# Kernel optimization log

Hardware: AMD Instinct MI355X
Metric: run time of the kernel (lower is better)

## Reference

```python
import jax, jax.numpy as jnp
import numpy as np


def setup_inputs() -> dict:
    key = jax.random.key(0)
    k1, k2 = jax.random.split(key)
    latent = jax.random.normal(k1, (131072, 128), dtype=jnp.float32)
    coords = jax.random.normal(k2, (2048, 128), dtype=jnp.float32)
    return {"latent": latent, "coords": coords}


def reference(latent, coords):
    # torch.cdist(latent, coords).min(1)[1]
    # argmin over euclidean distance == argmin over squared distance,
    # so we skip the sqrt (same result, cheaper and numerically safer).
    x2 = jnp.sum(latent * latent, axis=1, keepdims=True)          # [N, 1]
    c2 = jnp.sum(coords * coords, axis=1)                          # [C]
    cross = latent @ coords.T                                      # [N, C]
    d2 = x2 + c2[None, :] - 2.0 * cross                            # [N, C] squared dists
    return jnp.argmin(d2, axis=1)                                  # [N] int indices
```

## Files before the change

### kernel.cpp

```cpp
#include <hip/hip_runtime.h>


constexpr int D = 128;
constexpr int C = 2048;
constexpr int NCH = 64;
constexpr int NCHUNKS = C / NCH;
constexpr float MARGIN = 0.02f;
constexpr int WL_CAP = 32768;

constexpr size_t WS_CNT = 8192;
constexpr size_t WS_WL  = 16384;
constexpr size_t WS_BH  = 262144;
constexpr size_t WS_BL  = 786432;

typedef __attribute__((ext_vector_type(8))) short short8;
typedef __attribute__((ext_vector_type(4))) float f32x4;

__device__ inline unsigned short bf16_rne(float x) {
    unsigned u = __float_as_uint(x);
    u += 0x7FFFu + ((u >> 16) & 1u);
    return (unsigned short)(u >> 16);
}
__device__ inline float bf16_to_f(unsigned short h) {
    return __uint_as_float(((unsigned)h) << 16);
}
__device__ inline void split8(const float* v, short8* hi, short8* lo) {
#pragma unroll
    for (int j = 0; j < 8; ++j) {
        unsigned short h = bf16_rne(v[j]);
        (*hi)[j] = (short)h;
        (*lo)[j] = (short)bf16_rne(v[j] - bf16_to_f(h));
    }
}

__global__ void prep_coords(const float* __restrict__ coords,
                            unsigned short* __restrict__ Bh,
                            unsigned short* __restrict__ Bl,
                            float* __restrict__ c2, int* __restrict__ counter) {
    int t = blockIdx.x * blockDim.x + threadIdx.x;
    if (t == 0) *counter = 0;
    if (t >= C * 16) return;
    int c  = t >> 4;
    int k8 = t & 15;
    float v[8];
    *(float4*)(v)     = *(const float4*)(coords + (size_t)c * D + k8 * 8);
    *(float4*)(v + 4) = *(const float4*)(coords + (size_t)c * D + k8 * 8 + 4);
    short8 hi, lo;
    split8(v, &hi, &lo);
    int ch = c >> 6, nl = c & 63;
    size_t off = (size_t)ch * (NCH * 128) + ((size_t)nl * 16 + (k8 ^ (nl & 15))) * 8;
    *(short8*)(Bh + off) = hi;
    *(short8*)(Bl + off) = lo;
    float p = 0.f;
#pragma unroll
    for (int j = 0; j < 8; ++j) p = fmaf(v[j], v[j], p);
#pragma unroll
    for (int m = 1; m <= 8; m <<= 1) p += __shfl_xor(p, m, 64);
    if (k8 == 0) c2[c] = p;
}


__global__ __launch_bounds__(256, 3) void centroid_fast(
        const float* __restrict__ latent,
        const unsigned short* __restrict__ Bh_img,
        const unsigned short* __restrict__ Bl_img,
        const float* __restrict__ c2g,
        int* __restrict__ out,
        int* __restrict__ counter,
        int* __restrict__ worklist) {
    __shared__ __align__(16) unsigned short Bh[NCH * 128], Bl[NCH * 128];
    __shared__ float sc2[NCH];

    const int tid  = threadIdx.x;
    const int wid  = tid >> 6;
    const int lane = tid & 63;
    const int q    = lane >> 4, lr = lane & 15;
    const int row_block = blockIdx.x * 128;

    short8 Ah[2][4], Al[2][4];
#pragma unroll
    for (int mt = 0; mt < 2; ++mt) {
        const float* rp = latent + (size_t)(row_block + wid * 32 + mt * 16 + lr) * D;
#pragma unroll
        for (int ks = 0; ks < 4; ++ks) {
            float v[8];
            *(float4*)(v)     = *(const float4*)(rp + ks * 32 + q * 8);
            *(float4*)(v + 4) = *(const float4*)(rp + ks * 32 + q * 8 + 4);
            split8(v, &Ah[mt][ks], &Al[mt][ks]);
        }
    }

    float b1[8], b2[8];
    int   bidx[8];
#pragma unroll
    for (int s = 0; s < 8; ++s) { b1[s] = 3.4e38f; b2[s] = 3.4e38f; bidx[s] = 0; }

    for (int ch = 0; ch < NCHUNKS; ++ch) {
        __syncthreads();
        {
            const unsigned short* sh = Bh_img + (size_t)ch * (NCH * 128);
            const unsigned short* sl = Bl_img + (size_t)ch * (NCH * 128);
#pragma unroll
            for (int i = 0; i < 4; ++i) {
                int e = (i * 256 + tid) * 8;
                *(short8*)(Bh + e) = *(const short8*)(sh + e);
                *(short8*)(Bl + e) = *(const short8*)(sl + e);
            }
            if (tid < NCH) sc2[tid] = c2g[ch * NCH + tid];
        }
        __syncthreads();

#pragma unroll
        for (int nt = 0; nt < 4; ++nt) {
            const int nl = nt * 16 + lr;
            f32x4 acc[2];
#pragma unroll
            for (int mt = 0; mt < 2; ++mt) acc[mt] = (f32x4){0.f, 0.f, 0.f, 0.f};
#pragma unroll
            for (int ks = 0; ks < 4; ++ks) {
                const int xv = ((ks * 4) | q) ^ lr;
                const int e  = nl * 128 + xv * 8;
                short8 bh = *(const short8*)(Bh + e);
                short8 bl = *(const short8*)(Bl + e);
#pragma unroll
                for (int mt = 0; mt < 2; ++mt) {
                    acc[mt] = __builtin_amdgcn_mfma_f32_16x16x32_bf16(Ah[mt][ks], bh, acc[mt], 0, 0, 0);
                    acc[mt] = __builtin_amdgcn_mfma_f32_16x16x32_bf16(Ah[mt][ks], bl, acc[mt], 0, 0, 0);
                    acc[mt] = __builtin_amdgcn_mfma_f32_16x16x32_bf16(Al[mt][ks], bh, acc[mt], 0, 0, 0);
                }
            }
            const float c2v = sc2[nl];
            const int n_global = ch * NCH + nl;
#pragma unroll
            for (int mt = 0; mt < 2; ++mt)
#pragma unroll
                for (int r = 0; r < 4; ++r) {
                    int slot = mt * 4 + r;
                    float s = fmaf(-2.f, acc[mt][r], c2v);
                    bool lt = s < b1[slot];
                    float t = fmaxf(s, b1[slot]);
                    b2[slot]   = fminf(b2[slot], t);
                    b1[slot]   = fminf(s, b1[slot]);
                    bidx[slot] = lt ? n_global : bidx[slot];
                }
        }
    }

#pragma unroll
    for (int m = 1; m <= 8; m <<= 1) {
#pragma unroll
        for (int s = 0; s < 8; ++s) {
            float ob1 = __shfl_xor(b1[s], m, 64);
            float ob2 = __shfl_xor(b2[s], m, 64);
            int   oix = __shfl_xor(bidx[s], m, 64);
            float mx  = fmaxf(b1[s], ob1);
            b2[s] = fminf(fminf(b2[s], ob2), mx);
            bool take = (ob1 < b1[s]) || (ob1 == b1[s] && oix < bidx[s]);
            b1[s]   = take ? ob1 : b1[s];
            bidx[s] = take ? oix : bidx[s];
        }
    }
#pragma unroll
    for (int s = 0; s < 8; ++s) {
        if (lr == s) {
            int row = row_block + wid * 32 + (s >> 2) * 16 + q * 4 + (s & 3);
            out[row] = bidx[s];
            if (b2[s] - b1[s] < MARGIN) {
                int w = atomicAdd(counter, 1);
                if (w < WL_CAP) worklist[w] = row;
            }
        }
    }
}


__global__ __launch_bounds__(256) void refine_fp64(
        const float* __restrict__ latent, const float* __restrict__ coords,
        const int* __restrict__ worklist, const int* __restrict__ counter,
        int wl_cap, int* __restrict__ out) {
    __shared__ float  xs[D];
    __shared__ double rv[256];
    __shared__ int    ri[256];

    int n = *counter;
    if (n > wl_cap) n = wl_cap;

    for (int wi = blockIdx.x; wi < n; wi += gridDim.x) {
        int row = worklist[wi];
        if (threadIdx.x < D)
            xs[threadIdx.x] = latent[(size_t)row * D + threadIdx.x];
        __syncthreads();

        double best = 1.0e300;
        int    bix  = 0;
        for (int c = threadIdx.x; c < C; c += 256) {
            const float4* cp = (const float4*)(coords + (size_t)c * D);
            double s = 0.0;
#pragma unroll 8
            for (int k4 = 0; k4 < 32; ++k4) {
                float4 v = cp[k4];
                double d0 = (double)xs[k4 * 4 + 0] - (double)v.x;
                double d1 = (double)xs[k4 * 4 + 1] - (double)v.y;
                double d2 = (double)xs[k4 * 4 + 2] - (double)v.z;
                double d3 = (double)xs[k4 * 4 + 3] - (double)v.w;
                s = fma(d0, d0, s); s = fma(d1, d1, s);
                s = fma(d2, d2, s); s = fma(d3, d3, s);
            }
            if (s < best) { best = s; bix = c; }
        }
        rv[threadIdx.x] = best;
        ri[threadIdx.x] = bix;
        __syncthreads();
        for (int off = 128; off > 0; off >>= 1) {
            if (threadIdx.x < off) {
                double ov = rv[threadIdx.x + off];
                int    oi = ri[threadIdx.x + off];
                if (ov < rv[threadIdx.x] ||
                    (ov == rv[threadIdx.x] && oi < ri[threadIdx.x])) {
                    rv[threadIdx.x] = ov;
                    ri[threadIdx.x] = oi;
                }
            }
            __syncthreads();
        }
        if (threadIdx.x == 0) out[row] = ri[0];
        __syncthreads();
    }
}

extern "C" void kernel_launch(void* const* d_in, const int* in_sizes, int n_in,
                              void* d_out, int out_size, void* d_ws, size_t ws_size,
                              hipStream_t stream) {
    const float* latent = (const float*)d_in[0];
    const float* coords = (const float*)d_in[1];
    int*         out    = (int*)d_out;

    char* ws = (char*)d_ws;
    float* c2      = (float*)ws;
    int*   counter = (int*)(ws + WS_CNT);
    int*   wl      = (int*)(ws + WS_WL);
    unsigned short* Bh = (unsigned short*)(ws + WS_BH);
    unsigned short* Bl = (unsigned short*)(ws + WS_BL);
    const int n_rows = in_sizes[0] / D;

    prep_coords<<<(C * 16) / 256, 256, 0, stream>>>(coords, Bh, Bl, c2, counter);
    centroid_fast<<<n_rows / 128, 256, 0, stream>>>(latent, Bh, Bl, c2, out,
                                                    counter, wl);
    refine_fp64<<<608, 256, 0, stream>>>(latent, coords, wl, counter, WL_CAP, out);
}
```

Baseline: 327.3 us.

## Double-buffer coord chunks in LDS and batch four rows per refine block

The main kernel now uses two LDS buffers with half-size chunks of 32 centroids. The next chunk is prefetched into registers while the current one is computed, which removes one barrier per iteration and hides global-load latency behind MFMA work. The fp64 refine kernel now processes four worklist rows per block, reusing each coords load across four rows, and its grid shrinks from 608 to 256 blocks. This adds register pressure and more serial reductions per block, which may hurt occupancy at launch bound 3.

New measurement: 345.4 us. 1.06x slower.

```diff
diff --git a/kernel.cpp b/kernel.cpp
--- a/kernel.cpp
+++ b/kernel.cpp
@@ -3,7 +3,7 @@
 
 constexpr int D = 128;
 constexpr int C = 2048;
-constexpr int NCH = 64;
+constexpr int NCH = 32;
 constexpr int NCHUNKS = C / NCH;
 constexpr float MARGIN = 0.02f;
 constexpr int WL_CAP = 32768;
@@ -47,7 +47,7 @@
     *(float4*)(v + 4) = *(const float4*)(coords + (size_t)c * D + k8 * 8 + 4);
     short8 hi, lo;
     split8(v, &hi, &lo);
-    int ch = c >> 6, nl = c & 63;
+    int ch = c >> 5, nl = c & 31;
     size_t off = (size_t)ch * (NCH * 128) + ((size_t)nl * 16 + (k8 ^ (nl & 15))) * 8;
     *(short8*)(Bh + off) = hi;
     *(short8*)(Bl + off) = lo;
@@ -68,8 +68,8 @@
         int* __restrict__ out,
         int* __restrict__ counter,
         int* __restrict__ worklist) {
-    __shared__ __align__(16) unsigned short Bh[NCH * 128], Bl[NCH * 128];
-    __shared__ float sc2[NCH];
+    __shared__ __align__(16) unsigned short Bs[2][2][NCH * 128];
+    __shared__ float sc2[2][NCH];
 
     const int tid  = threadIdx.x;
     const int wid  = tid >> 6;
@@ -90,38 +90,50 @@
         }
     }
 
+#pragma unroll
+    for (int i = 0; i < 2; ++i) {
+        int o = (i * 256 + tid) * 8;
+        *(short8*)(&Bs[0][0][o]) = *(const short8*)(Bh_img + o);
+        *(short8*)(&Bs[0][1][o]) = *(const short8*)(Bl_img + o);
+    }
+    if (tid < NCH) sc2[0][tid] = c2g[tid];
+
     float b1[8], b2[8];
     int   bidx[8];
 #pragma unroll
     for (int s = 0; s < 8; ++s) { b1[s] = 3.4e38f; b2[s] = 3.4e38f; bidx[s] = 0; }
 
+    int buf = 0;
     for (int ch = 0; ch < NCHUNKS; ++ch) {
         __syncthreads();
-        {
-            const unsigned short* sh = Bh_img + (size_t)ch * (NCH * 128);
-            const unsigned short* sl = Bl_img + (size_t)ch * (NCH * 128);
-#pragma unroll
-            for (int i = 0; i < 4; ++i) {
-                int e = (i * 256 + tid) * 8;
-                *(short8*)(Bh + e) = *(const short8*)(sh + e);
-                *(short8*)(Bl + e) = *(const short8*)(sl + e);
-            }
-            if (tid < NCH) sc2[tid] = c2g[ch * NCH + tid];
-        }
-        __syncthreads();
-
-#pragma unroll
-        for (int nt = 0; nt < 4; ++nt) {
-            const int nl = nt * 16 + lr;
+
+        short8 nh[2], nlo[2];
+        float  nc2 = 0.f;
+        const bool more = (ch + 1 < NCHUNKS);
+        if (more) {
+            const unsigned short* sh = Bh_img + (size_t)(ch + 1) * (NCH * 128);
+            const unsigned short* sl = Bl_img + (size_t)(ch + 1) * (NCH * 128);
+#pragma unroll
+            for (int i = 0; i < 2; ++i) {
+                int o = (i * 256 + tid) * 8;
+                nh[i]  = *(const short8*)(sh + o);
+                nlo[i] = *(const short8*)(sl + o);
+            }
+            if (tid < NCH) nc2 = c2g[(ch + 1) * NCH + tid];
+        }
+
+#pragma unroll
+        for (int nt = 0; nt < 2; ++nt) {
+            const int nlc = nt * 16 + lr;
             f32x4 acc[2];
 #pragma unroll
             for (int mt = 0; mt < 2; ++mt) acc[mt] = (f32x4){0.f, 0.f, 0.f, 0.f};
 #pragma unroll
             for (int ks = 0; ks < 4; ++ks) {
                 const int xv = ((ks * 4) | q) ^ lr;
-                const int e  = nl * 128 + xv * 8;
-                short8 bh = *(const short8*)(Bh + e);
-                short8 bl = *(const short8*)(Bl + e);
+                const int e  = nlc * 128 + xv * 8;
+                short8 bh = *(const short8*)(&Bs[buf][0][e]);
+                short8 bl = *(const short8*)(&Bs[buf][1][e]);
 #pragma unroll
                 for (int mt = 0; mt < 2; ++mt) {
                     acc[mt] = __builtin_amdgcn_mfma_f32_16x16x32_bf16(Ah[mt][ks], bh, acc[mt], 0, 0, 0);
@@ -129,8 +141,8 @@
                     acc[mt] = __builtin_amdgcn_mfma_f32_16x16x32_bf16(Al[mt][ks], bh, acc[mt], 0, 0, 0);
                 }
             }
-            const float c2v = sc2[nl];
-            const int n_global = ch * NCH + nl;
+            const float c2v = sc2[buf][nlc];
+            const int n_global = ch * NCH + nlc;
 #pragma unroll
             for (int mt = 0; mt < 2; ++mt)
 #pragma unroll
@@ -144,6 +156,17 @@
                     bidx[slot] = lt ? n_global : bidx[slot];
                 }
         }
+
+        if (more) {
+#pragma unroll
+            for (int i = 0; i < 2; ++i) {
+                int o = (i * 256 + tid) * 8;
+                *(short8*)(&Bs[buf ^ 1][0][o]) = nh[i];
+                *(short8*)(&Bs[buf ^ 1][1][o]) = nlo[i];
+            }
+            if (tid < NCH) sc2[buf ^ 1][tid] = nc2;
+        }
+        buf ^= 1;
     }
 
 #pragma unroll
@@ -178,53 +201,71 @@
         const float* __restrict__ latent, const float* __restrict__ coords,
         const int* __restrict__ worklist, const int* __restrict__ counter,
         int wl_cap, int* __restrict__ out) {
-    __shared__ float  xs[D];
+    __shared__ float4 xs4[4][32];
     __shared__ double rv[256];
     __shared__ int    ri[256];
-
+    __shared__ int    rows_s[4];
+
+    const int tid = threadIdx.x;
     int n = *counter;
     if (n > wl_cap) n = wl_cap;
 
-    for (int wi = blockIdx.x; wi < n; wi += gridDim.x) {
-        int row = worklist[wi];
-        if (threadIdx.x < D)
-            xs[threadIdx.x] = latent[(size_t)row * D + threadIdx.x];
-        __syncthreads();
-
-        double best = 1.0e300;
-        int    bix  = 0;
-        for (int c = threadIdx.x; c < C; c += 256) {
+    for (int g0 = blockIdx.x * 4; g0 < n; g0 += gridDim.x * 4) {
+        int nr = n - g0; if (nr > 4) nr = 4;
+        __syncthreads();
+        if (tid < nr) rows_s[tid] = worklist[g0 + tid];
+        __syncthreads();
+        for (int i = tid; i < nr * 32; i += 256) {
+            int j = i >> 5, k4 = i & 31;
+            xs4[j][k4] = *(const float4*)(latent + (size_t)rows_s[j] * D + k4 * 4);
+        }
+        __syncthreads();
+
+        double best[4];
+        int    bix[4];
+#pragma unroll
+        for (int j = 0; j < 4; ++j) { best[j] = 1.0e300; bix[j] = 0; }
+
+        for (int c = tid; c < C; c += 256) {
             const float4* cp = (const float4*)(coords + (size_t)c * D);
-            double s = 0.0;
-#pragma unroll 8
+            double s[4] = {0.0, 0.0, 0.0, 0.0};
+#pragma unroll 4
             for (int k4 = 0; k4 < 32; ++k4) {
                 float4 v = cp[k4];
-                double d0 = (double)xs[k4 * 4 + 0] - (double)v.x;
-                double d1 = (double)xs[k4 * 4 + 1] - (double)v.y;
-                double d2 = (double)xs[k4 * 4 + 2] - (double)v.z;
-                double d3 = (double)xs[k4 * 4 + 3] - (double)v.w;
-                s = fma(d0, d0, s); s = fma(d1, d1, s);
-                s = fma(d2, d2, s); s = fma(d3, d3, s);
-            }
-            if (s < best) { best = s; bix = c; }
-        }
-        rv[threadIdx.x] = best;
-        ri[threadIdx.x] = bix;
-        __syncthreads();
-        for (int off = 128; off > 0; off >>= 1) {
-            if (threadIdx.x < off) {
-                double ov = rv[threadIdx.x + off];
-                int    oi = ri[threadIdx.x + off];
-                if (ov < rv[threadIdx.x] ||
-                    (ov == rv[threadIdx.x] && oi < ri[threadIdx.x])) {
-                    rv[threadIdx.x] = ov;
-                    ri[threadIdx.x] = oi;
-                }
-            }
+#pragma unroll
+                for (int j = 0; j < 4; ++j) {
+                    float4 x = xs4[j][k4];
+                    double d0 = (double)x.x - (double)v.x;
+                    double d1 = (double)x.y - (double)v.y;
+                    double d2 = (double)x.z - (double)v.z;
+                    double d3 = (double)x.w - (double)v.w;
+                    s[j] = fma(d0, d0, s[j]); s[j] = fma(d1, d1, s[j]);
+                    s[j] = fma(d2, d2, s[j]); s[j] = fma(d3, d3, s[j]);
+                }
+            }
+#pragma unroll
+            for (int j = 0; j < 4; ++j)
+                if (s[j] < best[j]) { best[j] = s[j]; bix[j] = c; }
+        }
+
+        for (int j = 0; j < 4; ++j) {
+            if (j >= nr) break;
+            rv[tid] = best[j];
+            ri[tid] = bix[j];
             __syncthreads();
-        }
-        if (threadIdx.x == 0) out[row] = ri[0];
-        __syncthreads();
+            for (int off = 128; off > 0; off >>= 1) {
+                if (tid < off) {
+                    double ov = rv[tid + off];
+                    int    oi = ri[tid + off];
+                    if (ov < rv[tid] || (ov == rv[tid] && oi < ri[tid])) {
+                        rv[tid] = ov; ri[tid] = oi;
+                    }
+                }
+                __syncthreads();
+            }
+            if (tid == 0) out[rows_s[j]] = ri[0];
+            __syncthreads();
+        }
     }
 }
 
@@ -246,5 +287,5 @@
     prep_coords<<<(C * 16) / 256, 256, 0, stream>>>(coords, Bh, Bl, c2, counter);
     centroid_fast<<<n_rows / 128, 256, 0, stream>>>(latent, Bh, Bl, c2, out,
                                                     counter, wl);
-    refine_fp64<<<608, 256, 0, stream>>>(latent, coords, wl, counter, WL_CAP, out);
-}
+    refine_fp64<<<256, 256, 0, stream>>>(latent, coords, wl, counter, WL_CAP, out);
+}
```
